# Kernel tuning notes

Measured on AMD Instinct MI355X. Metric: run time of the kernel, lower is better.

## Reference

```python
import jax, jax.numpy as jnp
import numpy as np

H, DH = 8, 64          # num_heads, head_dim
DM = H * DH            # hidden_dim = 512
LAM = 1.0              # lambda_param
SCALE = 1.0 / np.sqrt(DH)


def setup_inputs() -> dict:
    key = jax.random.key(0)
    ks = jax.random.split(key, 12)
    B, N, R = 2, 2048, 16
    s = DM ** -0.5
    inp = {
        "x": jax.random.normal(ks[0], (B, N, DM), jnp.float32),
        "pde_residuals": jax.random.normal(ks[1], (B, N, R), jnp.float32),
        "mask": jnp.ones((B, 1, N, N), jnp.int32),
        "Wq": jax.random.normal(ks[2], (DM, DM), jnp.float32) * s,
        "bq": jax.random.normal(ks[3], (DM,), jnp.float32) * 0.01,
        "Wk": jax.random.normal(ks[4], (DM, DM), jnp.float32) * s,
        "bk": jax.random.normal(ks[5], (DM,), jnp.float32) * 0.01,
        "Wv": jax.random.normal(ks[6], (DM, DM), jnp.float32) * s,
        "bv": jax.random.normal(ks[7], (DM,), jnp.float32) * 0.01,
        "Wo": jax.random.normal(ks[8], (DM, DM), jnp.float32) * s,
        "bo": jax.random.normal(ks[9], (DM,), jnp.float32) * 0.01,
    }
    return inp


def reference(x, pde_residuals, mask, Wq, bq, Wk, bk, Wv, bv, Wo, bo):
    B, N, _ = x.shape
    # torch nn.Linear: y = x @ W.T + b
    q = (x @ Wq.T + bq).reshape(B, N, H, DH)
    k = (x @ Wk.T + bk).reshape(B, N, H, DH)
    v = (x @ Wv.T + bv).reshape(B, N, H, DH)
    # [B,H,N,N]
    scores = jnp.einsum('bqhd,bkhd->bhqk', q, k) * SCALE
    # residual bias: rb.unsqueeze(1) - rb.unsqueeze(2) -> bias[b,i,j] = rb[b,j] - rb[b,i]
    rb = jnp.linalg.norm(pde_residuals, axis=-1)            # [B,N]
    bias = rb[:, None, None, :] - rb[:, None, :, None]       # [B,1,N,N]
    scores = scores - LAM * bias
    scores = jnp.where(mask == 0, -jnp.inf, scores)
    attn = jax.nn.softmax(scores, axis=-1)                   # dropout is identity in eval
    out = jnp.einsum('bhqk,bkhd->bqhd', attn, v).reshape(B, N, DM)
    return out @ Wo.T + bo
```

## Files before the change

### kernel.cpp

```cpp
#include <hip/hip_runtime.h>
#include <hip/hip_bf16.h>
#include <math.h>

#define B_ 2
#define N_ 2048
#define H_ 8
#define DH_ 64
#define DM_ 512
#define R_ 16
#define LAM_ 1.0f
#define SCALE_ 0.125f

typedef unsigned short u16;
typedef unsigned int u32;
typedef u16 u16x4 __attribute__((ext_vector_type(4)));
typedef u16 u16x8 __attribute__((ext_vector_type(8)));
typedef __bf16 bf16x8 __attribute__((ext_vector_type(8)));
typedef float f32x4 __attribute__((ext_vector_type(4)));

static __device__ __forceinline__ u16 f2bf(float f) {
    union { float f; unsigned u; } v; v.f = f;
    unsigned r = v.u + 0x7FFF + ((v.u >> 16) & 1);
    return (u16)(r >> 16);
}

static __device__ __forceinline__ u32 pack_bf16(float lo, float hi) {
    float2 f2; f2.x = lo; f2.y = hi;
    __hip_bfloat162 h2 = __float22bfloat162_rn(f2);
    u32 r;
    __builtin_memcpy(&r, &h2, 4);
    return r;
}

static __device__ __forceinline__ void gl_lds16(const void* g, void* l) {
    __builtin_amdgcn_global_load_lds(
        (const __attribute__((address_space(1))) unsigned*)g,
        (__attribute__((address_space(3))) unsigned*)l, 16, 0, 0);
}

__global__ __launch_bounds__(256) void cast_all(
    const float* __restrict__ x, const float* __restrict__ wq,
    const float* __restrict__ wk, const float* __restrict__ wv,
    const float* __restrict__ wo, u16* __restrict__ xb, u16* __restrict__ wqb,
    u16* __restrict__ wkb, u16* __restrict__ wvb, u16* __restrict__ wob) {
    int y = blockIdx.y;
    const float* src; u16* dst; int n;
    switch (y) {
        case 0: src = x;  dst = xb;  n = 2097152; break;
        case 1: src = wq; dst = wqb; n = 262144;  break;
        case 2: src = wk; dst = wkb; n = 262144;  break;
        case 3: src = wv; dst = wvb; n = 262144;  break;
        default: src = wo; dst = wob; n = 262144; break;
    }
    int i = (blockIdx.x * 256 + threadIdx.x) * 8;
    if (i >= n) return;
    float4 a = *(const float4*)(src + i);
    float4 b = *(const float4*)(src + i + 4);
    u16x8 o;
    o[0] = f2bf(a.x); o[1] = f2bf(a.y); o[2] = f2bf(a.z); o[3] = f2bf(a.w);
    o[4] = f2bf(b.x); o[5] = f2bf(b.y); o[6] = f2bf(b.z); o[7] = f2bf(b.w);
    *(u16x8*)(dst + i) = o;
}

__global__ void rb_kernel(const float* __restrict__ pde, float* __restrict__ rbs) {
    int i = blockIdx.x * blockDim.x + threadIdx.x;
    if (i >= B_ * N_) return;
    const float4* p = (const float4*)(pde + (size_t)i * R_);
    float s = 0.f;
#pragma unroll
    for (int j = 0; j < 4; ++j) {
        float4 v = p[j];
        s += v.x * v.x + v.y * v.y + v.z * v.z + v.w * v.w;
    }
    rbs[i] = LAM_ * sqrtf(s);
}

__global__ __launch_bounds__(256) void mask_scan(const int* __restrict__ mask,
                                                 int* __restrict__ flags) {
    int kt = blockIdx.x, qt = blockIdx.y, b = blockIdx.z;
    __shared__ int red;
    if (threadIdx.x == 0) red = 0;
    __syncthreads();
    int any = 0;
    for (int c = threadIdx.x; c < 1024; c += 256) {
        int row = c >> 4, seg = c & 15;
        int4 m4 = *(const int4*)(mask + (size_t)b * N_ * N_ +
                                 (size_t)(qt * 64 + row) * N_ + kt * 64 + seg * 4);
        any |= (m4.x == 0) | (m4.y == 0) | (m4.z == 0) | (m4.w == 0);
    }
    if (__ballot(any)) {
        if ((threadIdx.x & 63) == 0) atomicOr(&red, 1);
    }
    __syncthreads();
    if (threadIdx.x == 0) flags[(b * 32 + qt) * 32 + kt] = red;
}

struct Acc { f32x4 v[2][2]; };

static __device__ __forceinline__ Acc gemm_core(const u16* __restrict__ A,
                                                const u16* __restrict__ W,
                                                int m0, int nn0, char* LDSB) {
    int t = threadIdx.x, l = t & 63, w = t >> 6;
    int lg = l >> 4, li = l & 15;
    int wr = w >> 1, wc = w & 1;
    Acc acc;
#pragma unroll
    for (int m = 0; m < 2; ++m)
#pragma unroll
        for (int n = 0; n < 2; ++n) acc.v[m][n] = (f32x4){0.f, 0.f, 0.f, 0.f};

    int srow_l = l >> 3;
    int colb = ((l & 7) * 16) ^ (srow_l << 4);

    for (int k0 = 0; k0 < DM_; k0 += 64) {
        __syncthreads();
#pragma unroll
        for (int i = 0; i < 2; ++i) {
            int c = w * 2 + i;
            int row = c * 8 + srow_l;
            gl_lds16(A + (size_t)(m0 + row) * DM_ + k0 + (colb >> 1),
                     LDSB + c * 1024);
            gl_lds16(W + (size_t)(nn0 + row) * DM_ + k0 + (colb >> 1),
                     LDSB + 8192 + c * 1024);
        }
        __syncthreads();
#pragma unroll
        for (int kk = 0; kk < 2; ++kk) {
            bf16x8 af[2], bfr[2];
#pragma unroll
            for (int m = 0; m < 2; ++m) {
                int r = wr * 32 + m * 16 + li;
                af[m] = *(const bf16x8*)(LDSB + r * 128 +
                                         ((kk * 64 + lg * 16) ^ ((r & 7) << 4)));
            }
#pragma unroll
            for (int n = 0; n < 2; ++n) {
                int r = wc * 32 + n * 16 + li;
                bfr[n] = *(const bf16x8*)(LDSB + 8192 + r * 128 +
                                          ((kk * 64 + lg * 16) ^ ((r & 7) << 4)));
            }
#pragma unroll
            for (int m = 0; m < 2; ++m)
#pragma unroll
                for (int n = 0; n < 2; ++n)
                    acc.v[m][n] = __builtin_amdgcn_mfma_f32_16x16x32_bf16(
                        af[m], bfr[n], acc.v[m][n], 0, 0, 0);
        }
    }
    return acc;
}

__global__ __launch_bounds__(256) void gemm_qkv(
    const u16* __restrict__ xb, const u16* __restrict__ wqb,
    const u16* __restrict__ wkb, const u16* __restrict__ wvb,
    const float* __restrict__ bq, const float* __restrict__ bk,
    const float* __restrict__ bv, u16* __restrict__ q_bf,
    u16* __restrict__ k_bf, u16* __restrict__ vt) {
    __shared__ char LDSB[24576];
    int y = blockIdx.y;
    int which = y >> 3;
    int nn0 = (y & 7) * 64;
    const u16* W = which == 0 ? wqb : which == 1 ? wkb : wvb;
    const float* bias = which == 0 ? bq : which == 1 ? bk : bv;
    int m0 = blockIdx.x * 64;
    Acc acc = gemm_core(xb, W, m0, nn0, LDSB);

    int t = threadIdx.x, l = t & 63, w = t >> 6;
    int lg = l >> 4, li = l & 15;
    int wr = w >> 1, wc = w & 1;
    float scale = which == 0 ? SCALE_ : 1.0f;
#pragma unroll
    for (int n = 0; n < 2; ++n) {
        int col = nn0 + wc * 32 + n * 16 + li;
        float bv_ = bias[col];
        if (which < 2) {
            u16* dst = which == 0 ? q_bf : k_bf;
#pragma unroll
            for (int m = 0; m < 2; ++m)
#pragma unroll
                for (int r = 0; r < 4; ++r) {
                    int row = m0 + wr * 32 + m * 16 + lg * 4 + r;
                    dst[(size_t)row * DM_ + col] =
                        f2bf((acc.v[m][n][r] + bv_) * scale);
                }
        } else {
            int h = col >> 6, d = col & 63;
#pragma unroll
            for (int m = 0; m < 2; ++m) {
                int row = m0 + wr * 32 + m * 16 + lg * 4;
                int b = row >> 11, nb = row & (N_ - 1);
                u16x4 o;
#pragma unroll
                for (int r = 0; r < 4; ++r) o[r] = f2bf(acc.v[m][n][r] + bv_);
                *(u16x4*)(vt + ((size_t)((b * 8 + h) * 64 + d)) * N_ + nb) = o;
            }
        }
    }
}

__global__ __launch_bounds__(256) void gemm_out(
    const u16* __restrict__ aob, const u16* __restrict__ wob,
    const float* __restrict__ bo, float* __restrict__ out) {
    __shared__ char LDSB[24576];
    int nn0 = blockIdx.y * 64;
    int m0 = blockIdx.x * 64;
    Acc acc = gemm_core(aob, wob, m0, nn0, LDSB);

    int t = threadIdx.x, l = t & 63, w = t >> 6;
    int lg = l >> 4, li = l & 15;
    int wr = w >> 1, wc = w & 1;
#pragma unroll
    for (int n = 0; n < 2; ++n) {
        int col = nn0 + wc * 32 + n * 16 + li;
        float bv_ = bo[col];
#pragma unroll
        for (int m = 0; m < 2; ++m)
#pragma unroll
            for (int r = 0; r < 4; ++r) {
                int row = m0 + wr * 32 + m * 16 + lg * 4 + r;
                out[(size_t)row * DM_ + col] = acc.v[m][n][r] + bv_;
            }
    }
}

__global__ __launch_bounds__(512) void attn9(
    const u16* __restrict__ qb, const u16* __restrict__ kb,
    const u16* __restrict__ vtb, const float* __restrict__ rbs,
    const int* __restrict__ mask, const int* __restrict__ flags,
    u16* __restrict__ aob) {
    __shared__ char KVB[2][2][8192];
    __shared__ char PsB[8][1024];

    int t = threadIdx.x, l = t & 63, w = t >> 6;
    int g2 = w >> 2, wq = w & 3;
    int raw = blockIdx.x;
    int sid = (raw & 7) * 64 + (raw >> 3);
    int bh = sid >> 5, qg = sid & 31;
    int b = bh >> 3, h = bh & 7;
    int m0 = qg * 64 + wq * 16;
    int lg = l >> 4, li = l & 15;
    int k0base = g2 * 1024;

    int srl = l >> 3;
    int colb = ((l & 7) * 16) ^ (srl << 4);
    int vsrc_u = (l & 7) ^ srl;

    bf16x8 qa[2];
    {
        const u16* qrow = qb + (size_t)(b * N_ + m0 + li) * DM_ + h * DH_;
        qa[0] = __builtin_bit_cast(bf16x8, *(const u16x8*)(qrow + lg * 8));
        qa[1] = __builtin_bit_cast(bf16x8, *(const u16x8*)(qrow + 32 + lg * 8));
    }

    f32x4 o[4];
#pragma unroll
    for (int dt = 0; dt < 4; ++dt) o[dt] = (f32x4){0.f, 0.f, 0.f, 0.f};
    float mrun = -INFINITY, lrun = 0.f;

    auto STAGE = [&](int bufi, int k0s) {
        char* base = &KVB[g2][bufi][0];
        int row = wq * 8 + srl;
        gl_lds16(kb + (size_t)(b * N_ + k0s + row) * DM_ + h * DH_ + (colb >> 1),
                 base + wq * 1024);
        gl_lds16(vtb + ((size_t)(bh * DH_ + row * 2 + (vsrc_u >> 2))) * N_ +
                     k0s + (vsrc_u & 3) * 8,
                 base + 4096 + wq * 1024);
    };

    STAGE(0, k0base);
    __syncthreads();

    char* pwbase = &PsB[w][0] + li * 16 + ((lg & 1) << 3);
    int slot_lo = lg >> 1;
    int vfoff = ((li & 1) * 64 + lg * 16) ^ ((li >> 1) << 4);

    int buf = 0;
    for (int tt = 0; tt < 32; ++tt) {
        int k0 = k0base + tt * 32;
        if (tt < 31) STAGE(buf ^ 1, k0 + 32);

        const char* Kb = &KVB[g2][buf][0];
        const char* Vb = &KVB[g2][buf][4096];
        int flag = flags[(b * 32 + qg) * 32 + (k0 >> 6)];

        f32x4 st[2];
        __builtin_amdgcn_s_setprio(1);
#pragma unroll
        for (int kt = 0; kt < 2; ++kt) {
            st[kt] = (f32x4){0.f, 0.f, 0.f, 0.f};
#pragma unroll
            for (int s = 0; s < 2; ++s) {
                int key = kt * 16 + li;
                bf16x8 kf = *(const bf16x8*)(Kb + key * 128 +
                                             ((s * 64 + lg * 16) ^ ((key & 7) << 4)));
                st[kt] = __builtin_amdgcn_mfma_f32_16x16x32_bf16(kf, qa[s], st[kt],
                                                                 0, 0, 0);
            }
        }
        __builtin_amdgcn_s_setprio(0);

#pragma unroll
        for (int kt = 0; kt < 2; ++kt) {
            float4 rb4 = *(const float4*)(rbs + b * N_ + k0 + kt * 16 + lg * 4);
            st[kt][0] -= rb4.x; st[kt][1] -= rb4.y;
            st[kt][2] -= rb4.z; st[kt][3] -= rb4.w;
        }
        if (flag) {
#pragma unroll
            for (int kt = 0; kt < 2; ++kt)
#pragma unroll
                for (int r = 0; r < 4; ++r) {
                    int rowg = m0 + li;
                    int keyg = k0 + kt * 16 + lg * 4 + r;
                    if (mask[(size_t)b * N_ * N_ + (size_t)rowg * N_ + keyg] == 0)
                        st[kt][r] = -INFINITY;
                }
        }

        float mymax = fmaxf(
            fmaxf(fmaxf(st[0][0], st[0][1]), fmaxf(st[0][2], st[0][3])),
            fmaxf(fmaxf(st[1][0], st[1][1]), fmaxf(st[1][2], st[1][3])));
        if (!__all(mymax - mrun <= 8.0f)) {
            float pmax = mymax;
            pmax = fmaxf(pmax, __shfl_xor(pmax, 16));
            pmax = fmaxf(pmax, __shfl_xor(pmax, 32));
            float mnew = fmaxf(fmaxf(mrun, pmax), -3.0e38f);
            float corr = __expf(mrun - mnew);
            mrun = mnew;
            lrun *= corr;
#pragma unroll
            for (int dt = 0; dt < 4; ++dt)
#pragma unroll
                for (int r = 0; r < 4; ++r) o[dt][r] *= corr;
        }

#pragma unroll
        for (int kt = 0; kt < 2; ++kt) {
            float p0 = __expf(st[kt][0] - mrun);
            float p1 = __expf(st[kt][1] - mrun);
            float p2 = __expf(st[kt][2] - mrun);
            float p3 = __expf(st[kt][3] - mrun);
            lrun += (p0 + p1) + (p2 + p3);
            uint2 pkw;
            pkw.x = pack_bf16(p0, p1);
            pkw.y = pack_bf16(p2, p3);
            *(uint2*)(pwbase + ((kt * 2 + slot_lo) << 8)) = pkw;
        }

        bf16x8 pf = *(const bf16x8*)(&PsB[w][0] + (lg << 8) + li * 16);
        __builtin_amdgcn_s_setprio(1);
#pragma unroll
        for (int dt = 0; dt < 4; ++dt) {
            bf16x8 vf = *(const bf16x8*)(Vb + (dt * 8 + (li >> 1)) * 128 + vfoff);
            o[dt] = __builtin_amdgcn_mfma_f32_16x16x32_bf16(vf, pf, o[dt],
                                                            0, 0, 0);
        }
        __builtin_amdgcn_s_setprio(0);

        __syncthreads();
        buf ^= 1;
    }

    lrun += __shfl_xor(lrun, 16);
    lrun += __shfl_xor(lrun, 32);

    float* cmb = (float*)&KVB[0][0][0];
    float* mlc = (float*)&PsB[0][0];
    if (g2 == 1) {
        float* dst = cmb + wq * 1024;
#pragma unroll
        for (int dt = 0; dt < 4; ++dt)
            *(f32x4*)(dst + li * 64 + dt * 16 + lg * 4) = o[dt];
        if (lg == 0) {
            float2 ml; ml.x = mrun; ml.y = lrun;
            *(float2*)(mlc + (wq * 16 + li) * 2) = ml;
        }
    }
    __syncthreads();
    if (g2 == 0) {
        float2 ml1 = *(const float2*)(mlc + (wq * 16 + li) * 2);
        float m = fmaxf(mrun, ml1.x);
        float w0 = __expf(mrun - m), w1 = __expf(ml1.x - m);
        float denom = 1.f / (lrun * w0 + ml1.y * w1);
        w0 *= denom; w1 *= denom;
        const float* src = cmb + wq * 1024;
        u16* orow = aob + (size_t)(b * N_ + m0 + li) * DM_ + h * DH_;
#pragma unroll
        for (int dt = 0; dt < 4; ++dt) {
            f32x4 p1 = *(const f32x4*)(src + li * 64 + dt * 16 + lg * 4);
            u16x4 ov;
#pragma unroll
            for (int r = 0; r < 4; ++r)
                ov[r] = f2bf(o[dt][r] * w0 + p1[r] * w1);
            *(u16x4*)(orow + dt * 16 + lg * 4) = ov;
        }
    }
}

extern "C" void kernel_launch(void* const* d_in, const int* in_sizes, int n_in,
                              void* d_out, int out_size, void* d_ws, size_t ws_size,
                              hipStream_t stream) {
    const float* x   = (const float*)d_in[0];
    const float* pde = (const float*)d_in[1];
    const int*   msk = (const int*)d_in[2];
    const float* Wq  = (const float*)d_in[3];
    const float* bq  = (const float*)d_in[4];
    const float* Wk  = (const float*)d_in[5];
    const float* bk  = (const float*)d_in[6];
    const float* Wv  = (const float*)d_in[7];
    const float* bv  = (const float*)d_in[8];
    const float* Wo  = (const float*)d_in[9];
    const float* bo  = (const float*)d_in[10];
    float* out = (float*)d_out;

    const size_t MAT = (size_t)B_ * N_ * DM_;
    const size_t WSZ = (size_t)DM_ * DM_;
    u16* xb   = (u16*)d_ws;
    u16* q_bf = xb + MAT;
    u16* k_bf = q_bf + MAT;
    u16* vt   = k_bf + MAT;
    u16* aob  = vt + MAT;
    u16* wqb  = aob + MAT;
    u16* wkb  = wqb + WSZ;
    u16* wvb  = wkb + WSZ;
    u16* wob  = wvb + WSZ;
    float* rbs = (float*)(wob + WSZ);
    int* flags = (int*)(rbs + B_ * N_);

    cast_all<<<dim3(1024, 5), 256, 0, stream>>>(x, Wq, Wk, Wv, Wo,
                                                xb, wqb, wkb, wvb, wob);
    rb_kernel<<<(B_ * N_ + 255) / 256, 256, 0, stream>>>(pde, rbs);
    mask_scan<<<dim3(32, 32, 2), 256, 0, stream>>>(msk, flags);

    gemm_qkv<<<dim3(64, 24), 256, 0, stream>>>(xb, wqb, wkb, wvb,
                                               bq, bk, bv, q_bf, k_bf, vt);

    attn9<<<512, 512, 0, stream>>>(q_bf, k_bf, vt, rbs, msk, flags, aob);

    gemm_out<<<dim3(64, 8), 256, 0, stream>>>(aob, wob, bo, out);
}
```

Measured before the change: 82.62 us.

## Halve attention block query tile to 32 rows, doubling grid to 1024 blocks

Each attention block now handles 32 query rows with 4 waves (2 query halves by 2 key splits) instead of 64 rows with 8 waves, and the grid doubles to 1024 blocks. Each wave now issues two K/V staging loads per tile to fill the shared buffers. The aim is better load balance and occupancy across the 256 CUs with smaller blocks. In exchange, every K/V tile is loaded twice as often overall, which raises L2 and global traffic.

```diff
diff --git a/kernel.cpp b/kernel.cpp
--- a/kernel.cpp
+++ b/kernel.cpp
@@ -223,23 +223,23 @@
     }
 }
 
-__global__ __launch_bounds__(512) void attn9(
+__global__ __launch_bounds__(256) void attn10(
     const u16* __restrict__ qb, const u16* __restrict__ kb,
     const u16* __restrict__ vtb, const float* __restrict__ rbs,
     const int* __restrict__ mask, const int* __restrict__ flags,
     u16* __restrict__ aob) {
     __shared__ char KVB[2][2][8192];
-    __shared__ char PsB[8][1024];
+    __shared__ char PsB[4][1024];
 
     int t = threadIdx.x, l = t & 63, w = t >> 6;
-    int g2 = w >> 2, wq = w & 3;
+    int qh = w >> 1, ks = w & 1;
     int raw = blockIdx.x;
-    int sid = (raw & 7) * 64 + (raw >> 3);
-    int bh = sid >> 5, qg = sid & 31;
+    int sid = (raw & 7) * 128 + (raw >> 3);
+    int bh = sid >> 6, qg = sid & 63;
     int b = bh >> 3, h = bh & 7;
-    int m0 = qg * 64 + wq * 16;
+    int m0 = qg * 32 + qh * 16;
     int lg = l >> 4, li = l & 15;
-    int k0base = g2 * 1024;
+    int k0base = ks * 1024;
 
     int srl = l >> 3;
     int colb = ((l & 7) * 16) ^ (srl << 4);
@@ -258,13 +258,17 @@
     float mrun = -INFINITY, lrun = 0.f;
 
     auto STAGE = [&](int bufi, int k0s) {
-        char* base = &KVB[g2][bufi][0];
-        int row = wq * 8 + srl;
-        gl_lds16(kb + (size_t)(b * N_ + k0s + row) * DM_ + h * DH_ + (colb >> 1),
-                 base + wq * 1024);
-        gl_lds16(vtb + ((size_t)(bh * DH_ + row * 2 + (vsrc_u >> 2))) * N_ +
-                     k0s + (vsrc_u & 3) * 8,
-                 base + 4096 + wq * 1024);
+        char* base = &KVB[ks][bufi][0];
+#pragma unroll
+        for (int c = 0; c < 2; ++c) {
+            int cc = qh * 2 + c;
+            int row = cc * 8 + srl;
+            gl_lds16(kb + (size_t)(b * N_ + k0s + row) * DM_ + h * DH_ + (colb >> 1),
+                     base + cc * 1024);
+            gl_lds16(vtb + ((size_t)(bh * DH_ + row * 2 + (vsrc_u >> 2))) * N_ +
+                         k0s + (vsrc_u & 3) * 8,
+                     base + 4096 + cc * 1024);
+        }
     };
 
     STAGE(0, k0base);
@@ -279,9 +283,9 @@
         int k0 = k0base + tt * 32;
         if (tt < 31) STAGE(buf ^ 1, k0 + 32);
 
-        const char* Kb = &KVB[g2][buf][0];
-        const char* Vb = &KVB[g2][buf][4096];
-        int flag = flags[(b * 32 + qg) * 32 + (k0 >> 6)];
+        const char* Kb = &KVB[ks][buf][0];
+        const char* Vb = &KVB[ks][buf][4096];
+        int flag = flags[(b * 32 + (m0 >> 6)) * 32 + (k0 >> 6)];
 
         f32x4 st[2];
         __builtin_amdgcn_s_setprio(1);
@@ -366,24 +370,24 @@
 
     float* cmb = (float*)&KVB[0][0][0];
     float* mlc = (float*)&PsB[0][0];
-    if (g2 == 1) {
-        float* dst = cmb + wq * 1024;
+    if (ks == 1) {
+        float* dst = cmb + qh * 1024;
 #pragma unroll
         for (int dt = 0; dt < 4; ++dt)
             *(f32x4*)(dst + li * 64 + dt * 16 + lg * 4) = o[dt];
         if (lg == 0) {
             float2 ml; ml.x = mrun; ml.y = lrun;
-            *(float2*)(mlc + (wq * 16 + li) * 2) = ml;
+            *(float2*)(mlc + (qh * 16 + li) * 2) = ml;
         }
     }
     __syncthreads();
-    if (g2 == 0) {
-        float2 ml1 = *(const float2*)(mlc + (wq * 16 + li) * 2);
+    if (ks == 0) {
+        float2 ml1 = *(const float2*)(mlc + (qh * 16 + li) * 2);
         float m = fmaxf(mrun, ml1.x);
         float w0 = __expf(mrun - m), w1 = __expf(ml1.x - m);
         float denom = 1.f / (lrun * w0 + ml1.y * w1);
         w0 *= denom; w1 *= denom;
-        const float* src = cmb + wq * 1024;
+        const float* src = cmb + qh * 1024;
         u16* orow = aob + (size_t)(b * N_ + m0 + li) * DM_ + h * DH_;
 #pragma unroll
         for (int dt = 0; dt < 4; ++dt) {
@@ -435,7 +439,7 @@
     gemm_qkv<<<dim3(64, 24), 256, 0, stream>>>(xb, wqb, wkb, wvb,
                                                bq, bk, bv, q_bf, k_bf, vt);
 
-    attn9<<<512, 512, 0, stream>>>(q_bf, k_bf, vt, rbs, msk, flags, aob);
+    attn10<<<1024, 256, 0, stream>>>(q_bf, k_bf, vt, rbs, msk, flags, aob);
 
     gemm_out<<<dim3(64, 8), 256, 0, stream>>>(aob, wob, bo, out);
 }
```

Measured after the change: 89.06 us. 7.8% more time.
